# Kernel optimization log

Hardware: AMD Instinct MI355X
Metric: run time of the kernel (lower is better)

## Reference

```python
import jax, jax.numpy as jnp
import numpy as np

B, T, D, H, L = 128, 512, 512, 512, 2

def setup_inputs() -> dict:
    key = jax.random.key(0)
    k1, k2 = jax.random.split(key)
    x = jax.random.normal(k1, (B, T, D), dtype=jnp.float32)
    hiddens = jnp.zeros((L, 2, B, H), dtype=jnp.float32)  # [layer, (h,c), batch, hidden]
    # stacked per-layer fused-gate weights; torch Linear(in+hid, 4*hid)
    W = jax.random.normal(k2, (L, D + H, 4 * H), dtype=jnp.float32) * (1.0 / np.sqrt(D + H))
    b = jnp.zeros((L, 4 * H), dtype=jnp.float32)
    return {"x": x, "hiddens": hiddens, "W": W, "b": b}

def reference(x, hiddens, W, b):
    num_layers = W.shape[0]

    def step(hid, x_t):
        inp = x_t
        new = []
        for l in range(num_layers):
            h, c = hid[l, 0], hid[l, 1]
            gates = jnp.concatenate([inp, h], axis=-1) @ W[l] + b[l]  # [B, 4H]
            i, f, g, o = jnp.split(gates, 4, axis=-1)
            i = jax.nn.sigmoid(i)
            f = jax.nn.sigmoid(f)
            g = jnp.tanh(g)
            o = jax.nn.sigmoid(o)
            c_t = f * c + i * g
            h_t = o * jnp.tanh(c_t)
            new.append(jnp.stack([h_t, c_t], axis=0))
            inp = h_t
        hid = jnp.stack(new, axis=0)
        return hid, inp  # emit top-layer h per timestep

    hiddens_final, outs = jax.lax.scan(step, hiddens, jnp.swapaxes(x, 0, 1))
    outputs = jnp.swapaxes(outs, 0, 1)  # [B, T, H]
    return outputs, hiddens_final
```

## Files before the change

kernel.cpp:

```cpp
#include <hip/hip_runtime.h>
#include <stdint.h>

typedef __attribute__((ext_vector_type(4))) int   i32x4;
typedef __attribute__((ext_vector_type(8))) short bf16x8;
typedef __attribute__((ext_vector_type(4))) float f32x4;

#define DEV static __device__ __forceinline__

constexpr int  kB = 128, kT = 512, kD = 512, kH = 512;
constexpr int  kGC = 2048;
constexpr int  ROWS = 32;
constexpr int  NG = 4;
constexpr int  NJ = 32;
constexpr int  NTHREADS = 512;
constexpr size_t SLOT_ELEMS = (size_t)kB * kH;
constexpr size_t WIMG_ELEMS = (size_t)2 * NJ * 4 * 32 * 512;
constexpr size_t WIMG_BYTES = WIMG_ELEMS * 2;
constexpr int  RFULL = kT + 1;
constexpr int  FLAG_STRIDE = 128;
constexpr size_t FLAG_TOTAL = (size_t)2 * NG * kT * FLAG_STRIDE;
constexpr uint64_t ONE8 = 0x0101010101010101ull;

DEV ushort f2bf(float f) {
  uint32_t u = __float_as_uint(f);
  u += 0x7fff + ((u >> 16) & 1);
  return (ushort)(u >> 16);
}
DEV int pk2(float a, float b) { return (int)((uint32_t)f2bf(a) | ((uint32_t)f2bf(b) << 16)); }
DEV float sigf(float v)  { return 1.f / (1.f + __expf(-v)); }
DEV float tanhf_(float v){ return 1.f - 2.f / (__expf(2.f * v) + 1.f); }

DEV uint64_t ald64(const uint64_t* p) {
  return __hip_atomic_load(p, __ATOMIC_RELAXED, __HIP_MEMORY_SCOPE_AGENT);
}

DEV void poll32(const uint8_t* fb) {
  const uint64_t* p = reinterpret_cast<const uint64_t*>(fb);
  for (;;) {
    uint64_t a = ald64(p) & ald64(p + 1) & ald64(p + 2) & ald64(p + 3);
    if (a == ONE8) return;
    __builtin_amdgcn_s_sleep(1);
  }
}

__global__ void prep_w(const float* __restrict__ W, ushort* __restrict__ wimg) {
  uint32_t idx = blockIdx.x * 256u + threadIdx.x;
  int e = idx & 7, lane = (idx >> 3) & 63, ks = (idx >> 9) & 31;
  int G = (idx >> 14) & 3, j = (idx >> 16) & 31, l = (idx >> 21) & 1;
  int k = ks * 32 + ((lane >> 4) << 3) + e;
  int c = G * 512 + j * 16 + (lane & 15);
  wimg[idx] = f2bf(W[(size_t)l * 1024 * 2048 + (size_t)k * 2048 + c]);
}

__global__ void prep_init(const float* __restrict__ hiddens, ushort* __restrict__ r0, ushort* __restrict__ r1) {
  uint32_t idx = blockIdx.x * 256u + threadIdx.x;
  int l = idx >> 16; uint32_t r = idx & 65535u;
  ushort v = f2bf(hiddens[(size_t)(l * 2 + 0) * 65536 + r]);
  (l ? r1 : r0)[r] = v;
}

DEV void stage_h(ushort* Ab, const ushort* rbase, int g, int tid) {
  #pragma unroll
  for (int p = 0; p < 4; ++p) {
    int o = (tid + p * NTHREADS) * 16, row = o >> 10, kb = o & 1023;
    i32x4 v = *reinterpret_cast<const i32x4*>(rbase + (size_t)(g * ROWS + row) * kH + (kb >> 1));
    *reinterpret_cast<i32x4*>(reinterpret_cast<char*>(Ab) + ((row * 1024 + kb) ^ ((row & 7) << 4))) = v;
  }
}

DEV int gsw(int r, int c) { return r * 16 + (c ^ ((((r) >> 2) & 3) << 2)); }

__launch_bounds__(NTHREADS, 1)
__global__ void lstm_v7(const float* __restrict__ x, const float* __restrict__ hiddens,
                        const float* __restrict__ bias, const ushort* __restrict__ wimg,
                        ushort* __restrict__ ring0, ushort* __restrict__ ring1,
                        uint8_t* __restrict__ flags, float* __restrict__ out) {
  __shared__ ushort AbufX[ROWS * 512];
  __shared__ ushort AbufH[ROWS * 512];
  __shared__ float  gbuf[4][4][ROWS * 16];

  const int tid  = threadIdx.x;
  const int lane = tid & 63;
  const int wv   = tid >> 6;
  const int kq   = wv >> 1;
  const int Gp   = wv & 1;
  const int j    = blockIdx.x & 31;
  const int g    = (blockIdx.x >> 5) & 3;
  const int l    = blockIdx.x >> 7;

  __threadfence();

  i32x4 wrA[8], wrB[8];
  {
    const int GA = 2 * Gp, GB = 2 * Gp + 1;
    const ushort* baseA = wimg + (((size_t)(l * NJ + j) * 4 + GA) * 32) * 512 + lane * 8;
    const ushort* baseB = wimg + (((size_t)(l * NJ + j) * 4 + GB) * 32) * 512 + lane * 8;
    #pragma unroll
    for (int s = 0; s < 4; ++s) {
      wrA[s]     = *reinterpret_cast<const i32x4*>(baseA + (kq * 4 + s) * 512);
      wrA[4 + s] = *reinterpret_cast<const i32x4*>(baseA + (16 + kq * 4 + s) * 512);
      wrB[s]     = *reinterpret_cast<const i32x4*>(baseB + (kq * 4 + s) * 512);
      wrB[4 + s] = *reinterpret_cast<const i32x4*>(baseB + (16 + kq * 4 + s) * 512);
    }
  }
  const int urow = tid >> 4, ucol = tid & 15;
  const float b0 = bias[l * kGC + 0 * 512 + j * 16 + ucol];
  const float b1 = bias[l * kGC + 1 * 512 + j * 16 + ucol];
  const float b2 = bias[l * kGC + 2 * 512 + j * 16 + ucol];
  const float b3 = bias[l * kGC + 3 * 512 + j * 16 + ucol];
  float creg = hiddens[((size_t)(l * 2 + 1) * kB + (g * ROWS + urow)) * kH + j * 16 + ucol];

  ushort* rrec = l ? ring1 : ring0;
  uint8_t* myflags = flags + (size_t)(l * NG + g) * kT * FLAG_STRIDE;
  const uint8_t* xflags = flags + (size_t)g * kT * FLAG_STRIDE;

  const int koff   = (lane >> 4) << 3;
  const int abase0 = (lane & 15) * 1024;
  const int abase1 = abase0 + 16 * 1024;
  const int aswz   = (lane & 7) << 4;
  const int uswz   = gsw(urow, ucol);

  f32x4 xr[8];
  if (l == 0) {
    #pragma unroll
    for (int p = 0; p < 4; ++p) {
      int o = (tid + p * NTHREADS) * 16, row = o >> 10, kb = o & 1023;
      const float* src = x + ((size_t)(g * ROWS + row) * kT + 0) * kD + (kb >> 1);
      xr[2 * p]     = *reinterpret_cast<const f32x4*>(src);
      xr[2 * p + 1] = *reinterpret_cast<const f32x4*>(src + 4);
    }
  }

  for (int t = 0; t < kT; ++t) {
    if (l == 0) {
      #pragma unroll
      for (int p = 0; p < 4; ++p) {
        int o = (tid + p * NTHREADS) * 16, row = o >> 10, kb = o & 1023;
        i32x4 v;
        v[0] = pk2(xr[2 * p][0], xr[2 * p][1]);         v[1] = pk2(xr[2 * p][2], xr[2 * p][3]);
        v[2] = pk2(xr[2 * p + 1][0], xr[2 * p + 1][1]); v[3] = pk2(xr[2 * p + 1][2], xr[2 * p + 1][3]);
        *reinterpret_cast<i32x4*>(reinterpret_cast<char*>(AbufX) + ((row * 1024 + kb) ^ ((row & 7) << 4))) = v;
      }
    } else {
      poll32(xflags + (size_t)t * FLAG_STRIDE);
      stage_h(AbufX, ring0 + (size_t)(t + 1) * SLOT_ELEMS, g, tid);
    }
    __syncthreads();

    if (l == 0 && t + 1 < kT) {
      #pragma unroll
      for (int p = 0; p < 4; ++p) {
        int o = (tid + p * NTHREADS) * 16, row = o >> 10, kb = o & 1023;
        const float* src = x + ((size_t)(g * ROWS + row) * kT + (t + 1)) * kD + (kb >> 1);
        xr[2 * p]     = *reinterpret_cast<const f32x4*>(src);
        xr[2 * p + 1] = *reinterpret_cast<const f32x4*>(src + 4);
      }
    }

    f32x4 a0r0 = {}, a0r1 = {}, a1r0 = {}, a1r1 = {};
    #pragma unroll
    for (int s = 0; s < 4; ++s) {
      int kb = ((kq * 4 + s) * 32 + koff) << 1;
      i32x4 av0 = *reinterpret_cast<const i32x4*>(reinterpret_cast<const char*>(AbufX) + ((abase0 + kb) ^ aswz));
      i32x4 av1 = *reinterpret_cast<const i32x4*>(reinterpret_cast<const char*>(AbufX) + ((abase1 + kb) ^ aswz));
      a0r0 = __builtin_amdgcn_mfma_f32_16x16x32_bf16(
               *reinterpret_cast<bf16x8*>(&av0), *reinterpret_cast<bf16x8*>(&wrA[s]), a0r0, 0, 0, 0);
      a1r0 = __builtin_amdgcn_mfma_f32_16x16x32_bf16(
               *reinterpret_cast<bf16x8*>(&av0), *reinterpret_cast<bf16x8*>(&wrB[s]), a1r0, 0, 0, 0);
      a0r1 = __builtin_amdgcn_mfma_f32_16x16x32_bf16(
               *reinterpret_cast<bf16x8*>(&av1), *reinterpret_cast<bf16x8*>(&wrA[s]), a0r1, 0, 0, 0);
      a1r1 = __builtin_amdgcn_mfma_f32_16x16x32_bf16(
               *reinterpret_cast<bf16x8*>(&av1), *reinterpret_cast<bf16x8*>(&wrB[s]), a1r1, 0, 0, 0);
    }

    if (t > 0) poll32(myflags + (size_t)(t - 1) * FLAG_STRIDE);
    stage_h(AbufH, rrec + (size_t)t * SLOT_ELEMS, g, tid);
    __syncthreads();

    #pragma unroll
    for (int s = 0; s < 4; ++s) {
      int kb = ((kq * 4 + s) * 32 + koff) << 1;
      i32x4 av0 = *reinterpret_cast<const i32x4*>(reinterpret_cast<const char*>(AbufH) + ((abase0 + kb) ^ aswz));
      i32x4 av1 = *reinterpret_cast<const i32x4*>(reinterpret_cast<const char*>(AbufH) + ((abase1 + kb) ^ aswz));
      a0r0 = __builtin_amdgcn_mfma_f32_16x16x32_bf16(
               *reinterpret_cast<bf16x8*>(&av0), *reinterpret_cast<bf16x8*>(&wrA[4 + s]), a0r0, 0, 0, 0);
      a1r0 = __builtin_amdgcn_mfma_f32_16x16x32_bf16(
               *reinterpret_cast<bf16x8*>(&av0), *reinterpret_cast<bf16x8*>(&wrB[4 + s]), a1r0, 0, 0, 0);
      a0r1 = __builtin_amdgcn_mfma_f32_16x16x32_bf16(
               *reinterpret_cast<bf16x8*>(&av1), *reinterpret_cast<bf16x8*>(&wrA[4 + s]), a0r1, 0, 0, 0);
      a1r1 = __builtin_amdgcn_mfma_f32_16x16x32_bf16(
               *reinterpret_cast<bf16x8*>(&av1), *reinterpret_cast<bf16x8*>(&wrB[4 + s]), a1r1, 0, 0, 0);
    }

    #pragma unroll
    for (int q = 0; q < 4; ++q) {
      int r0 = ((lane >> 4) << 2) + q;
      int c  = lane & 15;
      gbuf[kq][2 * Gp + 0][gsw(r0, c)]      = a0r0[q];
      gbuf[kq][2 * Gp + 1][gsw(r0, c)]      = a1r0[q];
      gbuf[kq][2 * Gp + 0][gsw(r0 + 16, c)] = a0r1[q];
      gbuf[kq][2 * Gp + 1][gsw(r0 + 16, c)] = a1r1[q];
    }
    __syncthreads();

    float hh;
    {
      float si = gbuf[0][0][uswz] + gbuf[1][0][uswz] + gbuf[2][0][uswz] + gbuf[3][0][uswz];
      float sf = gbuf[0][1][uswz] + gbuf[1][1][uswz] + gbuf[2][1][uswz] + gbuf[3][1][uswz];
      float sg = gbuf[0][2][uswz] + gbuf[1][2][uswz] + gbuf[2][2][uswz] + gbuf[3][2][uswz];
      float so = gbuf[0][3][uswz] + gbuf[1][3][uswz] + gbuf[2][3][uswz] + gbuf[3][3][uswz];
      float iv = sigf(si + b0);
      float fv = sigf(sf + b1);
      float gv = tanhf_(sg + b2);
      float ov = sigf(so + b3);
      creg = fv * creg + iv * gv;
      hh = ov * tanhf_(creg);
      uint32_t me    = f2bf(hh);
      uint32_t other = (uint32_t)__shfl_xor((int)me, 1);
      if (!(ucol & 1)) {
        uint32_t pkv = me | (other << 16);
        uint32_t* dst = (uint32_t*)(rrec + (size_t)(t + 1) * SLOT_ELEMS
                                    + (size_t)(g * ROWS + urow) * kH + j * 16 + ucol);
        __hip_atomic_store(dst, pkv, __ATOMIC_RELAXED, __HIP_MEMORY_SCOPE_AGENT);
      }
    }
    asm volatile("s_waitcnt vmcnt(0)" ::: "memory");
    __syncthreads();
    if (tid == 0)
      __hip_atomic_store(myflags + (size_t)t * FLAG_STRIDE + j, (uint8_t)1,
                         __ATOMIC_RELAXED, __HIP_MEMORY_SCOPE_AGENT);

    {
      int b = g * ROWS + urow;
      if (l == 1) out[((size_t)b * kT + t) * kH + j * 16 + ucol] = hh;
      if (t == kT - 1) {
        size_t hb = (size_t)kB * kT * kH;
        out[hb + ((size_t)(l * 2 + 0) * kB + b) * kH + j * 16 + ucol] = hh;
        out[hb + ((size_t)(l * 2 + 1) * kB + b) * kH + j * 16 + ucol] = creg;
      }
    }
  }
}


template<bool BIG>
DEV void stage_ring(ushort* Abuf_, const ushort* rbase, int g, int tid) {
  #pragma unroll
  for (int p = 0; p < 4; ++p) {
    int o = (tid + p * NTHREADS) * 16;
    int row = o >> 10, kb = o & 1023;
    const ushort* src = rbase + (size_t)(g * ROWS + row) * kH + (kb >> 1);
    i32x4 v;
    if (BIG) {
      v = *reinterpret_cast<const i32x4*>(src);
    } else {
      uint64_t lo = __hip_atomic_load((const uint64_t*)src,       __ATOMIC_RELAXED, __HIP_MEMORY_SCOPE_AGENT);
      uint64_t hi = __hip_atomic_load((const uint64_t*)(src + 4), __ATOMIC_RELAXED, __HIP_MEMORY_SCOPE_AGENT);
      v[0] = (int)(uint32_t)lo; v[1] = (int)(uint32_t)(lo >> 32);
      v[2] = (int)(uint32_t)hi; v[3] = (int)(uint32_t)(hi >> 32);
    }
    *reinterpret_cast<i32x4*>(reinterpret_cast<char*>(Abuf_) + ((row * 1024 + kb) ^ ((row & 7) << 4))) = v;
  }
}

template<bool BIG>
__launch_bounds__(NTHREADS, 2)
__global__ void lstm_main(const float* __restrict__ x, const float* __restrict__ hiddens,
                          const float* __restrict__ bias, const ushort* __restrict__ wimg,
                          ushort* __restrict__ ring0, ushort* __restrict__ ring1,
                          int* __restrict__ cnt, int* __restrict__ cons0,
                          float* __restrict__ out, int R0, int R1) {
  __shared__ ushort Abuf[ROWS * 512];
  __shared__ float  gbuf[4][ROWS][16];
  __shared__ float  cbuf[ROWS][16];
  __shared__ float  hbuf[ROWS][16];

  const int tid  = threadIdx.x;
  const int lane = tid & 63;
  const int wv   = tid >> 6;
  const int G    = wv & 3;
  const int rf   = wv >> 2;
  const int j    = blockIdx.x & 31;
  const int g    = (blockIdx.x >> 5) & 3;
  const int l    = blockIdx.x >> 7;

  __threadfence();

  i32x4 wr[32];
  {
    const ushort* base = wimg + (((size_t)(l * NJ + j) * 4 + G) * 32) * 512 + lane * 8;
    #pragma unroll
    for (int ks = 0; ks < 32; ++ks)
      wr[ks] = *reinterpret_cast<const i32x4*>(base + ks * 512);
  }
  const float bval = bias[l * kGC + G * 512 + j * 16 + (lane & 15)];
  {
    int row = tid >> 4, col = tid & 15;
    cbuf[row][col] = hiddens[((size_t)(l * 2 + 1) * kB + (g * ROWS + row)) * kH + j * 16 + col];
  }
  int* mycnt = cnt + (l * NG + g) * kT;
  int* c0cnt = cnt + g * kT;
  ushort* rrec = l ? ring1 : ring0;
  const int Rrec = l ? R1 : R0;

  const int arow  = rf * 16 + (lane & 15);
  const int koff  = (lane >> 4) << 3;
  const int abase = arow * 1024;
  const int aswz  = (arow & 7) << 4;

  __syncthreads();

  for (int t = 0; t < kT; ++t) {
    if (l == 1) {
      if (tid == 0) {
        while (__hip_atomic_load(&c0cnt[t], __ATOMIC_RELAXED, __HIP_MEMORY_SCOPE_AGENT) < NJ)
          __builtin_amdgcn_s_sleep(2);
      }
      __syncthreads();
      stage_ring<BIG>(Abuf, ring0 + (size_t)((t + 1) % R0) * SLOT_ELEMS, g, tid);
    } else {
      #pragma unroll
      for (int p = 0; p < 4; ++p) {
        int o = (tid + p * NTHREADS) * 16;
        int row = o >> 10, kb = o & 1023;
        const float* src = x + ((size_t)(g * ROWS + row) * kT + t) * kD + (kb >> 1);
        f32x4 f0 = *reinterpret_cast<const f32x4*>(src);
        f32x4 f1 = *reinterpret_cast<const f32x4*>(src + 4);
        i32x4 v;
        v[0] = pk2(f0[0], f0[1]); v[1] = pk2(f0[2], f0[3]);
        v[2] = pk2(f1[0], f1[1]); v[3] = pk2(f1[2], f1[3]);
        *reinterpret_cast<i32x4*>(reinterpret_cast<char*>(Abuf) + ((row * 1024 + kb) ^ ((row & 7) << 4))) = v;
      }
    }
    __syncthreads();
    if (!BIG && l == 1 && tid == 0)
      __hip_atomic_fetch_add(&cons0[g * kT + t], 1, __ATOMIC_RELAXED, __HIP_MEMORY_SCOPE_AGENT);

    f32x4 acc = {};
    #pragma unroll
    for (int ks = 0; ks < 16; ++ks) {
      int off = (abase + ((ks * 32 + koff) << 1)) ^ aswz;
      i32x4 av = *reinterpret_cast<const i32x4*>(reinterpret_cast<const char*>(Abuf) + off);
      acc = __builtin_amdgcn_mfma_f32_16x16x32_bf16(
              *reinterpret_cast<bf16x8*>(&av), *reinterpret_cast<bf16x8*>(&wr[ks]), acc, 0, 0, 0);
    }
    __syncthreads();

    if (t > 0) {
      if (tid == 0) {
        while (__hip_atomic_load(&mycnt[t - 1], __ATOMIC_RELAXED, __HIP_MEMORY_SCOPE_AGENT) < NJ)
          __builtin_amdgcn_s_sleep(2);
        if (!BIG && l == 0 && t >= R0) {
          while (__hip_atomic_load(&cons0[g * kT + (t - R0)], __ATOMIC_RELAXED, __HIP_MEMORY_SCOPE_AGENT) < NJ)
            __builtin_amdgcn_s_sleep(2);
        }
      }
      __syncthreads();
    }
    stage_ring<BIG>(Abuf, rrec + (size_t)(t % Rrec) * SLOT_ELEMS, g, tid);
    __syncthreads();

    #pragma unroll
    for (int ks = 0; ks < 16; ++ks) {
      int off = (abase + ((ks * 32 + koff) << 1)) ^ aswz;
      i32x4 av = *reinterpret_cast<const i32x4*>(reinterpret_cast<const char*>(Abuf) + off);
      acc = __builtin_amdgcn_mfma_f32_16x16x32_bf16(
              *reinterpret_cast<bf16x8*>(&av), *reinterpret_cast<bf16x8*>(&wr[16 + ks]), acc, 0, 0, 0);
    }

    #pragma unroll
    for (int q = 0; q < 4; ++q) {
      float v2 = acc[q] + bval;
      v2 = (G == 2) ? tanhf_(v2) : sigf(v2);
      gbuf[G][rf * 16 + ((lane >> 4) << 2) + q][lane & 15] = v2;
    }
    __syncthreads();

    {
      int row = tid >> 4, col = tid & 15;
      float iv = gbuf[0][row][col], fv = gbuf[1][row][col];
      float gv = gbuf[2][row][col], ov = gbuf[3][row][col];
      float cc = fv * cbuf[row][col] + iv * gv;
      cbuf[row][col] = cc;
      float hh = ov * tanhf_(cc);
      hbuf[row][col] = hh;
      int b = g * ROWS + row;
      if (l == 1) out[((size_t)b * kT + t) * kH + j * 16 + col] = hh;
      if (t == kT - 1) {
        size_t hb = (size_t)kB * kT * kH;
        out[hb + ((size_t)(l * 2 + 0) * kB + b) * kH + j * 16 + col] = hh;
        out[hb + ((size_t)(l * 2 + 1) * kB + b) * kH + j * 16 + col] = cc;
      }
    }
    __syncthreads();

    if (tid < 256) {
      int row = tid >> 3, cp = tid & 7;
      uint32_t pkv = (uint32_t)f2bf(hbuf[row][2 * cp]) | ((uint32_t)f2bf(hbuf[row][2 * cp + 1]) << 16);
      uint32_t* dst = (uint32_t*)(rrec + (size_t)((t + 1) % Rrec) * SLOT_ELEMS
                                  + (size_t)(g * ROWS + row) * kH + j * 16 + 2 * cp);
      __hip_atomic_store(dst, pkv, __ATOMIC_RELAXED, __HIP_MEMORY_SCOPE_AGENT);
    }
    asm volatile("s_waitcnt vmcnt(0)" ::: "memory");
    __syncthreads();
    if (tid == 0)
      __hip_atomic_fetch_add(&mycnt[t], 1, __ATOMIC_RELAXED, __HIP_MEMORY_SCOPE_AGENT);
  }
}

extern "C" void kernel_launch(void* const* d_in, const int* in_sizes, int n_in,
                              void* d_out, int out_size, void* d_ws, size_t ws_size,
                              hipStream_t stream) {
  const float* x  = (const float*)d_in[0];
  const float* hd = (const float*)d_in[1];
  const float* W  = (const float*)d_in[2];
  const float* b  = (const float*)d_in[3];
  float* out = (float*)d_out;

  char* ws = (char*)d_ws;
  ushort* wimg = (ushort*)ws;
  uint8_t* flags = (uint8_t*)(ws + WIMG_BYTES);
  int* cnt  = (int*)(ws + WIMG_BYTES + FLAG_TOTAL);
  int* cons = (int*)(ws + WIMG_BYTES + FLAG_TOTAL + 16384);
  size_t ringoff = WIMG_BYTES + FLAG_TOTAL + 32768;
  size_t avail = ws_size > ringoff ? ws_size - ringoff : 0;
  long rmax = (long)(avail / (2 * SLOT_ELEMS * 2));
  int R = (rmax >= RFULL) ? RFULL : (rmax >= 16 ? 16 : (rmax >= 2 ? (int)rmax : 2));
  ushort* ring0 = (ushort*)(ws + ringoff);
  ushort* ring1 = ring0 + (size_t)R * SLOT_ELEMS;

  prep_w<<<(int)(WIMG_ELEMS / 256), 256, 0, stream>>>(W, wimg);
  prep_init<<<(2 * kB * kH) / 256, 256, 0, stream>>>(hd, ring0, ring1);
  if (R == RFULL) {
    hipMemsetAsync(flags, 0, FLAG_TOTAL, stream);
    lstm_v7<<<256, NTHREADS, 0, stream>>>(x, hd, b, wimg, ring0, ring1, flags, out);
  } else {
    hipMemsetAsync(ws + WIMG_BYTES + FLAG_TOTAL, 0, 32768, stream);
    lstm_main<false><<<256, NTHREADS, 0, stream>>>(x, hd, b, wimg, ring0, ring1, cnt, cons, out, R, R);
  }
}
```

Measured before the change: 2.160 ms.

## Split batch into 16-row groups, doubling persistent blocks to 512

Batch groups shrink from 32 to 16 rows, giving 8 groups per layer and 512 persistent blocks instead of 256. Each block does half the MFMA and staging work per step, which shortens the per-timestep critical path on the serial recurrence. The cost is that every block loads the same register-resident weights, so weight traffic doubles, and flag synchronisation fans out more widely. Half the threads sit idle in the elementwise phase. The persistent scheme also needs all 512 blocks co-resident, which the launch bound of four blocks per CU is meant to allow.

```diff
diff --git a/kernel.cpp b/kernel.cpp
--- a/kernel.cpp
+++ b/kernel.cpp
@@ -10,7 +10,9 @@
 constexpr int  kB = 128, kT = 512, kD = 512, kH = 512;
 constexpr int  kGC = 2048;
 constexpr int  ROWS = 32;
+constexpr int  GROWS = 16;
 constexpr int  NG = 4;
+constexpr int  NGG = 8;
 constexpr int  NJ = 32;
 constexpr int  NTHREADS = 512;
 constexpr size_t SLOT_ELEMS = (size_t)kB * kH;
@@ -18,7 +20,7 @@
 constexpr size_t WIMG_BYTES = WIMG_ELEMS * 2;
 constexpr int  RFULL = kT + 1;
 constexpr int  FLAG_STRIDE = 128;
-constexpr size_t FLAG_TOTAL = (size_t)2 * NG * kT * FLAG_STRIDE;
+constexpr size_t FLAG_TOTAL = (size_t)2 * NGG * kT * FLAG_STRIDE;
 constexpr uint64_t ONE8 = 0x0101010101010101ull;
 
 DEV ushort f2bf(float f) {
@@ -59,25 +61,25 @@
   (l ? r1 : r0)[r] = v;
 }
 
-DEV void stage_h(ushort* Ab, const ushort* rbase, int g, int tid) {
+DEV void stage_h16(ushort* Ab, const ushort* rbase, int gg, int tid) {
   #pragma unroll
-  for (int p = 0; p < 4; ++p) {
+  for (int p = 0; p < 2; ++p) {
     int o = (tid + p * NTHREADS) * 16, row = o >> 10, kb = o & 1023;
-    i32x4 v = *reinterpret_cast<const i32x4*>(rbase + (size_t)(g * ROWS + row) * kH + (kb >> 1));
+    i32x4 v = *reinterpret_cast<const i32x4*>(rbase + (size_t)(gg * GROWS + row) * kH + (kb >> 1));
     *reinterpret_cast<i32x4*>(reinterpret_cast<char*>(Ab) + ((row * 1024 + kb) ^ ((row & 7) << 4))) = v;
   }
 }
 
 DEV int gsw(int r, int c) { return r * 16 + (c ^ ((((r) >> 2) & 3) << 2)); }
 
-__launch_bounds__(NTHREADS, 1)
-__global__ void lstm_v7(const float* __restrict__ x, const float* __restrict__ hiddens,
+__launch_bounds__(NTHREADS, 4)
+__global__ void lstm_v8(const float* __restrict__ x, const float* __restrict__ hiddens,
                         const float* __restrict__ bias, const ushort* __restrict__ wimg,
                         ushort* __restrict__ ring0, ushort* __restrict__ ring1,
                         uint8_t* __restrict__ flags, float* __restrict__ out) {
-  __shared__ ushort AbufX[ROWS * 512];
-  __shared__ ushort AbufH[ROWS * 512];
-  __shared__ float  gbuf[4][4][ROWS * 16];
+  __shared__ ushort AbufX[GROWS * 512];
+  __shared__ ushort AbufH[GROWS * 512];
+  __shared__ float  gbuf[4][4][GROWS * 16];
 
   const int tid  = threadIdx.x;
   const int lane = tid & 63;
@@ -85,8 +87,8 @@
   const int kq   = wv >> 1;
   const int Gp   = wv & 1;
   const int j    = blockIdx.x & 31;
-  const int g    = (blockIdx.x >> 5) & 3;
-  const int l    = blockIdx.x >> 7;
+  const int gg   = (blockIdx.x >> 5) & 7;
+  const int l    = blockIdx.x >> 8;
 
   __threadfence();
 
@@ -103,29 +105,31 @@
       wrB[4 + s] = *reinterpret_cast<const i32x4*>(baseB + (16 + kq * 4 + s) * 512);
     }
   }
-  const int urow = tid >> 4, ucol = tid & 15;
-  const float b0 = bias[l * kGC + 0 * 512 + j * 16 + ucol];
-  const float b1 = bias[l * kGC + 1 * 512 + j * 16 + ucol];
-  const float b2 = bias[l * kGC + 2 * 512 + j * 16 + ucol];
-  const float b3 = bias[l * kGC + 3 * 512 + j * 16 + ucol];
-  float creg = hiddens[((size_t)(l * 2 + 1) * kB + (g * ROWS + urow)) * kH + j * 16 + ucol];
+  const int urow = (tid >> 4) & 15, ucol = tid & 15;
+  float b0 = 0.f, b1 = 0.f, b2 = 0.f, b3 = 0.f, creg = 0.f;
+  if (tid < 256) {
+    b0 = bias[l * kGC + 0 * 512 + j * 16 + ucol];
+    b1 = bias[l * kGC + 1 * 512 + j * 16 + ucol];
+    b2 = bias[l * kGC + 2 * 512 + j * 16 + ucol];
+    b3 = bias[l * kGC + 3 * 512 + j * 16 + ucol];
+    creg = hiddens[((size_t)(l * 2 + 1) * kB + (gg * GROWS + urow)) * kH + j * 16 + ucol];
+  }
 
   ushort* rrec = l ? ring1 : ring0;
-  uint8_t* myflags = flags + (size_t)(l * NG + g) * kT * FLAG_STRIDE;
-  const uint8_t* xflags = flags + (size_t)g * kT * FLAG_STRIDE;
-
-  const int koff   = (lane >> 4) << 3;
-  const int abase0 = (lane & 15) * 1024;
-  const int abase1 = abase0 + 16 * 1024;
-  const int aswz   = (lane & 7) << 4;
-  const int uswz   = gsw(urow, ucol);
-
-  f32x4 xr[8];
+  uint8_t* myflags = flags + (size_t)(l * NGG + gg) * kT * FLAG_STRIDE;
+  const uint8_t* xflags = flags + (size_t)gg * kT * FLAG_STRIDE;
+
+  const int koff  = (lane >> 4) << 3;
+  const int abase = (lane & 15) * 1024;
+  const int aswz  = (lane & 7) << 4;
+  const int uswz  = gsw(urow, ucol);
+
+  f32x4 xr[4];
   if (l == 0) {
     #pragma unroll
-    for (int p = 0; p < 4; ++p) {
+    for (int p = 0; p < 2; ++p) {
       int o = (tid + p * NTHREADS) * 16, row = o >> 10, kb = o & 1023;
-      const float* src = x + ((size_t)(g * ROWS + row) * kT + 0) * kD + (kb >> 1);
+      const float* src = x + ((size_t)(gg * GROWS + row) * kT + 0) * kD + (kb >> 1);
       xr[2 * p]     = *reinterpret_cast<const f32x4*>(src);
       xr[2 * p + 1] = *reinterpret_cast<const f32x4*>(src + 4);
     }
@@ -134,7 +138,7 @@
   for (int t = 0; t < kT; ++t) {
     if (l == 0) {
       #pragma unroll
-      for (int p = 0; p < 4; ++p) {
+      for (int p = 0; p < 2; ++p) {
         int o = (tid + p * NTHREADS) * 16, row = o >> 10, kb = o & 1023;
         i32x4 v;
         v[0] = pk2(xr[2 * p][0], xr[2 * p][1]);         v[1] = pk2(xr[2 * p][2], xr[2 * p][3]);
@@ -143,68 +147,55 @@
       }
     } else {
       poll32(xflags + (size_t)t * FLAG_STRIDE);
-      stage_h(AbufX, ring0 + (size_t)(t + 1) * SLOT_ELEMS, g, tid);
+      stage_h16(AbufX, ring0 + (size_t)(t + 1) * SLOT_ELEMS, gg, tid);
     }
     __syncthreads();
 
     if (l == 0 && t + 1 < kT) {
       #pragma unroll
-      for (int p = 0; p < 4; ++p) {
+      for (int p = 0; p < 2; ++p) {
         int o = (tid + p * NTHREADS) * 16, row = o >> 10, kb = o & 1023;
-        const float* src = x + ((size_t)(g * ROWS + row) * kT + (t + 1)) * kD + (kb >> 1);
+        const float* src = x + ((size_t)(gg * GROWS + row) * kT + (t + 1)) * kD + (kb >> 1);
         xr[2 * p]     = *reinterpret_cast<const f32x4*>(src);
         xr[2 * p + 1] = *reinterpret_cast<const f32x4*>(src + 4);
       }
     }
 
-    f32x4 a0r0 = {}, a0r1 = {}, a1r0 = {}, a1r1 = {};
+    f32x4 a0 = {}, a1 = {};
     #pragma unroll
     for (int s = 0; s < 4; ++s) {
       int kb = ((kq * 4 + s) * 32 + koff) << 1;
-      i32x4 av0 = *reinterpret_cast<const i32x4*>(reinterpret_cast<const char*>(AbufX) + ((abase0 + kb) ^ aswz));
-      i32x4 av1 = *reinterpret_cast<const i32x4*>(reinterpret_cast<const char*>(AbufX) + ((abase1 + kb) ^ aswz));
-      a0r0 = __builtin_amdgcn_mfma_f32_16x16x32_bf16(
-               *reinterpret_cast<bf16x8*>(&av0), *reinterpret_cast<bf16x8*>(&wrA[s]), a0r0, 0, 0, 0);
-      a1r0 = __builtin_amdgcn_mfma_f32_16x16x32_bf16(
-               *reinterpret_cast<bf16x8*>(&av0), *reinterpret_cast<bf16x8*>(&wrB[s]), a1r0, 0, 0, 0);
-      a0r1 = __builtin_amdgcn_mfma_f32_16x16x32_bf16(
-               *reinterpret_cast<bf16x8*>(&av1), *reinterpret_cast<bf16x8*>(&wrA[s]), a0r1, 0, 0, 0);
-      a1r1 = __builtin_amdgcn_mfma_f32_16x16x32_bf16(
-               *reinterpret_cast<bf16x8*>(&av1), *reinterpret_cast<bf16x8*>(&wrB[s]), a1r1, 0, 0, 0);
+      i32x4 av = *reinterpret_cast<const i32x4*>(reinterpret_cast<const char*>(AbufX) + ((abase + kb) ^ aswz));
+      a0 = __builtin_amdgcn_mfma_f32_16x16x32_bf16(
+             *reinterpret_cast<bf16x8*>(&av), *reinterpret_cast<bf16x8*>(&wrA[s]), a0, 0, 0, 0);
+      a1 = __builtin_amdgcn_mfma_f32_16x16x32_bf16(
+             *reinterpret_cast<bf16x8*>(&av), *reinterpret_cast<bf16x8*>(&wrB[s]), a1, 0, 0, 0);
     }
 
     if (t > 0) poll32(myflags + (size_t)(t - 1) * FLAG_STRIDE);
-    stage_h(AbufH, rrec + (size_t)t * SLOT_ELEMS, g, tid);
+    stage_h16(AbufH, rrec + (size_t)t * SLOT_ELEMS, gg, tid);
     __syncthreads();
 
     #pragma unroll
     for (int s = 0; s < 4; ++s) {
       int kb = ((kq * 4 + s) * 32 + koff) << 1;
-      i32x4 av0 = *reinterpret_cast<const i32x4*>(reinterpret_cast<const char*>(AbufH) + ((abase0 + kb) ^ aswz));
-      i32x4 av1 = *reinterpret_cast<const i32x4*>(reinterpret_cast<const char*>(AbufH) + ((abase1 + kb) ^ aswz));
-      a0r0 = __builtin_amdgcn_mfma_f32_16x16x32_bf16(
-               *reinterpret_cast<bf16x8*>(&av0), *reinterpret_cast<bf16x8*>(&wrA[4 + s]), a0r0, 0, 0, 0);
-      a1r0 = __builtin_amdgcn_mfma_f32_16x16x32_bf16(
-               *reinterpret_cast<bf16x8*>(&av0), *reinterpret_cast<bf16x8*>(&wrB[4 + s]), a1r0, 0, 0, 0);
-      a0r1 = __builtin_amdgcn_mfma_f32_16x16x32_bf16(
-               *reinterpret_cast<bf16x8*>(&av1), *reinterpret_cast<bf16x8*>(&wrA[4 + s]), a0r1, 0, 0, 0);
-      a1r1 = __builtin_amdgcn_mfma_f32_16x16x32_bf16(
-               *reinterpret_cast<bf16x8*>(&av1), *reinterpret_cast<bf16x8*>(&wrB[4 + s]), a1r1, 0, 0, 0);
+      i32x4 av = *reinterpret_cast<const i32x4*>(reinterpret_cast<const char*>(AbufH) + ((abase + kb) ^ aswz));
+      a0 = __builtin_amdgcn_mfma_f32_16x16x32_bf16(
+             *reinterpret_cast<bf16x8*>(&av), *reinterpret_cast<bf16x8*>(&wrA[4 + s]), a0, 0, 0, 0);
+      a1 = __builtin_amdgcn_mfma_f32_16x16x32_bf16(
+             *reinterpret_cast<bf16x8*>(&av), *reinterpret_cast<bf16x8*>(&wrB[4 + s]), a1, 0, 0, 0);
     }
 
     #pragma unroll
     for (int q = 0; q < 4; ++q) {
-      int r0 = ((lane >> 4) << 2) + q;
-      int c  = lane & 15;
-      gbuf[kq][2 * Gp + 0][gsw(r0, c)]      = a0r0[q];
-      gbuf[kq][2 * Gp + 1][gsw(r0, c)]      = a1r0[q];
-      gbuf[kq][2 * Gp + 0][gsw(r0 + 16, c)] = a0r1[q];
-      gbuf[kq][2 * Gp + 1][gsw(r0 + 16, c)] = a1r1[q];
-    }
-    __syncthreads();
-
-    float hh;
-    {
+      int r = ((lane >> 4) << 2) + q, c = lane & 15;
+      gbuf[kq][2 * Gp + 0][gsw(r, c)] = a0[q];
+      gbuf[kq][2 * Gp + 1][gsw(r, c)] = a1[q];
+    }
+    __syncthreads();
+
+    float hh = 0.f;
+    if (tid < 256) {
       float si = gbuf[0][0][uswz] + gbuf[1][0][uswz] + gbuf[2][0][uswz] + gbuf[3][0][uswz];
       float sf = gbuf[0][1][uswz] + gbuf[1][1][uswz] + gbuf[2][1][uswz] + gbuf[3][1][uswz];
       float sg = gbuf[0][2][uswz] + gbuf[1][2][uswz] + gbuf[2][2][uswz] + gbuf[3][2][uswz];
@@ -220,7 +211,7 @@
       if (!(ucol & 1)) {
         uint32_t pkv = me | (other << 16);
         uint32_t* dst = (uint32_t*)(rrec + (size_t)(t + 1) * SLOT_ELEMS
-                                    + (size_t)(g * ROWS + urow) * kH + j * 16 + ucol);
+                                    + (size_t)(gg * GROWS + urow) * kH + j * 16 + ucol);
         __hip_atomic_store(dst, pkv, __ATOMIC_RELAXED, __HIP_MEMORY_SCOPE_AGENT);
       }
     }
@@ -230,8 +221,8 @@
       __hip_atomic_store(myflags + (size_t)t * FLAG_STRIDE + j, (uint8_t)1,
                          __ATOMIC_RELAXED, __HIP_MEMORY_SCOPE_AGENT);
 
-    {
-      int b = g * ROWS + urow;
+    if (tid < 256) {
+      int b = gg * GROWS + urow;
       if (l == 1) out[((size_t)b * kT + t) * kH + j * 16 + ucol] = hh;
       if (t == kT - 1) {
         size_t hb = (size_t)kB * kT * kH;
@@ -433,7 +424,7 @@
   prep_init<<<(2 * kB * kH) / 256, 256, 0, stream>>>(hd, ring0, ring1);
   if (R == RFULL) {
     hipMemsetAsync(flags, 0, FLAG_TOTAL, stream);
-    lstm_v7<<<256, NTHREADS, 0, stream>>>(x, hd, b, wimg, ring0, ring1, flags, out);
+    lstm_v8<<<512, NTHREADS, 0, stream>>>(x, hd, b, wimg, ring0, ring1, flags, out);
   } else {
     hipMemsetAsync(ws + WIMG_BYTES + FLAG_TOTAL, 0, 32768, stream);
     lstm_main<false><<<256, NTHREADS, 0, stream>>>(x, hd, b, wimg, ring0, ring1, cnt, cons, out, R, R);
```

New measurement: 2.331 ms. +7.9%, slower.

## Load MFMA A-operands directly from global into registers, dropping LDS staging

Applied to the files above, without the earlier changes.

Each wave now reads its own x and h MFMA fragments straight from global memory (the ring buffers or x) into registers, instead of the whole block cooperatively staging them into swizzled LDS buffers. This removes two __syncthreads per timestep along with the LDS write/read round trip on the serial recurrence path. In exchange each wave issues smaller, less coalesced global loads (16-byte chunks at row stride), there is redundant loading across waves sharing rows, and register pressure rises because of the larger x prefetch array.

```diff
diff --git a/kernel.cpp b/kernel.cpp
--- a/kernel.cpp
+++ b/kernel.cpp
@@ -59,25 +59,14 @@
   (l ? r1 : r0)[r] = v;
 }
 
-DEV void stage_h(ushort* Ab, const ushort* rbase, int g, int tid) {
-  #pragma unroll
-  for (int p = 0; p < 4; ++p) {
-    int o = (tid + p * NTHREADS) * 16, row = o >> 10, kb = o & 1023;
-    i32x4 v = *reinterpret_cast<const i32x4*>(rbase + (size_t)(g * ROWS + row) * kH + (kb >> 1));
-    *reinterpret_cast<i32x4*>(reinterpret_cast<char*>(Ab) + ((row * 1024 + kb) ^ ((row & 7) << 4))) = v;
-  }
-}
-
 DEV int gsw(int r, int c) { return r * 16 + (c ^ ((((r) >> 2) & 3) << 2)); }
 
 __launch_bounds__(NTHREADS, 1)
-__global__ void lstm_v7(const float* __restrict__ x, const float* __restrict__ hiddens,
+__global__ void lstm_v9(const float* __restrict__ x, const float* __restrict__ hiddens,
                         const float* __restrict__ bias, const ushort* __restrict__ wimg,
                         ushort* __restrict__ ring0, ushort* __restrict__ ring1,
                         uint8_t* __restrict__ flags, float* __restrict__ out) {
-  __shared__ ushort AbufX[ROWS * 512];
-  __shared__ ushort AbufH[ROWS * 512];
-  __shared__ float  gbuf[4][4][ROWS * 16];
+  __shared__ float gbuf[4][4][ROWS * 16];
 
   const int tid  = threadIdx.x;
   const int lane = tid & 63;
@@ -114,92 +103,90 @@
   uint8_t* myflags = flags + (size_t)(l * NG + g) * kT * FLAG_STRIDE;
   const uint8_t* xflags = flags + (size_t)g * kT * FLAG_STRIDE;
 
-  const int koff   = (lane >> 4) << 3;
-  const int abase0 = (lane & 15) * 1024;
-  const int abase1 = abase0 + 16 * 1024;
-  const int aswz   = (lane & 7) << 4;
-  const int uswz   = gsw(urow, ucol);
-
-  f32x4 xr[8];
+  const int r0 = lane & 15;
+  const int cb = (lane >> 4) << 3;
+  const int ksb = kq * 4;
+  const int uswz = gsw(urow, ucol);
+
+  f32x4 xpf[16];
   if (l == 0) {
-    #pragma unroll
-    for (int p = 0; p < 4; ++p) {
-      int o = (tid + p * NTHREADS) * 16, row = o >> 10, kb = o & 1023;
-      const float* src = x + ((size_t)(g * ROWS + row) * kT + 0) * kD + (kb >> 1);
-      xr[2 * p]     = *reinterpret_cast<const f32x4*>(src);
-      xr[2 * p + 1] = *reinterpret_cast<const f32x4*>(src + 4);
+    const float* xb0 = x + ((size_t)(g * ROWS + r0) * kT + 0) * kD + cb;
+    #pragma unroll
+    for (int f = 0; f < 8; ++f) {
+      const float* src = xb0 + (size_t)((f >> 2) * 16) * kT * kD + (ksb + (f & 3)) * 32;
+      xpf[2 * f]     = *reinterpret_cast<const f32x4*>(src);
+      xpf[2 * f + 1] = *reinterpret_cast<const f32x4*>(src + 4);
     }
   }
 
   for (int t = 0; t < kT; ++t) {
+    i32x4 xb[8];
     if (l == 0) {
       #pragma unroll
-      for (int p = 0; p < 4; ++p) {
-        int o = (tid + p * NTHREADS) * 16, row = o >> 10, kb = o & 1023;
+      for (int f = 0; f < 8; ++f) {
         i32x4 v;
-        v[0] = pk2(xr[2 * p][0], xr[2 * p][1]);         v[1] = pk2(xr[2 * p][2], xr[2 * p][3]);
-        v[2] = pk2(xr[2 * p + 1][0], xr[2 * p + 1][1]); v[3] = pk2(xr[2 * p + 1][2], xr[2 * p + 1][3]);
-        *reinterpret_cast<i32x4*>(reinterpret_cast<char*>(AbufX) + ((row * 1024 + kb) ^ ((row & 7) << 4))) = v;
+        v[0] = pk2(xpf[2 * f][0], xpf[2 * f][1]);         v[1] = pk2(xpf[2 * f][2], xpf[2 * f][3]);
+        v[2] = pk2(xpf[2 * f + 1][0], xpf[2 * f + 1][1]); v[3] = pk2(xpf[2 * f + 1][2], xpf[2 * f + 1][3]);
+        xb[f] = v;
+      }
+      if (t + 1 < kT) {
+        const float* xb0 = x + ((size_t)(g * ROWS + r0) * kT + (t + 1)) * kD + cb;
+        #pragma unroll
+        for (int f = 0; f < 8; ++f) {
+          const float* src = xb0 + (size_t)((f >> 2) * 16) * kT * kD + (ksb + (f & 3)) * 32;
+          xpf[2 * f]     = *reinterpret_cast<const f32x4*>(src);
+          xpf[2 * f + 1] = *reinterpret_cast<const f32x4*>(src + 4);
+        }
       }
     } else {
       poll32(xflags + (size_t)t * FLAG_STRIDE);
-      stage_h(AbufX, ring0 + (size_t)(t + 1) * SLOT_ELEMS, g, tid);
-    }
-    __syncthreads();
-
-    if (l == 0 && t + 1 < kT) {
+      const ushort* xs = ring0 + (size_t)(t + 1) * SLOT_ELEMS + (size_t)(g * ROWS + r0) * kH + cb;
       #pragma unroll
-      for (int p = 0; p < 4; ++p) {
-        int o = (tid + p * NTHREADS) * 16, row = o >> 10, kb = o & 1023;
-        const float* src = x + ((size_t)(g * ROWS + row) * kT + (t + 1)) * kD + (kb >> 1);
-        xr[2 * p]     = *reinterpret_cast<const f32x4*>(src);
-        xr[2 * p + 1] = *reinterpret_cast<const f32x4*>(src + 4);
-      }
+      for (int f = 0; f < 8; ++f)
+        xb[f] = *reinterpret_cast<const i32x4*>(xs + (size_t)((f >> 2) * 16) * kH + (ksb + (f & 3)) * 32);
     }
 
     f32x4 a0r0 = {}, a0r1 = {}, a1r0 = {}, a1r1 = {};
     #pragma unroll
     for (int s = 0; s < 4; ++s) {
-      int kb = ((kq * 4 + s) * 32 + koff) << 1;
-      i32x4 av0 = *reinterpret_cast<const i32x4*>(reinterpret_cast<const char*>(AbufX) + ((abase0 + kb) ^ aswz));
-      i32x4 av1 = *reinterpret_cast<const i32x4*>(reinterpret_cast<const char*>(AbufX) + ((abase1 + kb) ^ aswz));
       a0r0 = __builtin_amdgcn_mfma_f32_16x16x32_bf16(
-               *reinterpret_cast<bf16x8*>(&av0), *reinterpret_cast<bf16x8*>(&wrA[s]), a0r0, 0, 0, 0);
+               *reinterpret_cast<bf16x8*>(&xb[s]), *reinterpret_cast<bf16x8*>(&wrA[s]), a0r0, 0, 0, 0);
       a1r0 = __builtin_amdgcn_mfma_f32_16x16x32_bf16(
-               *reinterpret_cast<bf16x8*>(&av0), *reinterpret_cast<bf16x8*>(&wrB[s]), a1r0, 0, 0, 0);
+               *reinterpret_cast<bf16x8*>(&xb[s]), *reinterpret_cast<bf16x8*>(&wrB[s]), a1r0, 0, 0, 0);
       a0r1 = __builtin_amdgcn_mfma_f32_16x16x32_bf16(
-               *reinterpret_cast<bf16x8*>(&av1), *reinterpret_cast<bf16x8*>(&wrA[s]), a0r1, 0, 0, 0);
+               *reinterpret_cast<bf16x8*>(&xb[4 + s]), *reinterpret_cast<bf16x8*>(&wrA[s]), a0r1, 0, 0, 0);
       a1r1 = __builtin_amdgcn_mfma_f32_16x16x32_bf16(
-               *reinterpret_cast<bf16x8*>(&av1), *reinterpret_cast<bf16x8*>(&wrB[s]), a1r1, 0, 0, 0);
+               *reinterpret_cast<bf16x8*>(&xb[4 + s]), *reinterpret_cast<bf16x8*>(&wrB[s]), a1r1, 0, 0, 0);
     }
 
     if (t > 0) poll32(myflags + (size_t)(t - 1) * FLAG_STRIDE);
-    stage_h(AbufH, rrec + (size_t)t * SLOT_ELEMS, g, tid);
-    __syncthreads();
+    i32x4 hr[8];
+    {
+      const ushort* hs = rrec + (size_t)t * SLOT_ELEMS + (size_t)(g * ROWS + r0) * kH + cb;
+      #pragma unroll
+      for (int f = 0; f < 8; ++f)
+        hr[f] = *reinterpret_cast<const i32x4*>(hs + (size_t)((f >> 2) * 16) * kH + (ksb + (f & 3)) * 32);
+    }
 
     #pragma unroll
     for (int s = 0; s < 4; ++s) {
-      int kb = ((kq * 4 + s) * 32 + koff) << 1;
-      i32x4 av0 = *reinterpret_cast<const i32x4*>(reinterpret_cast<const char*>(AbufH) + ((abase0 + kb) ^ aswz));
-      i32x4 av1 = *reinterpret_cast<const i32x4*>(reinterpret_cast<const char*>(AbufH) + ((abase1 + kb) ^ aswz));
       a0r0 = __builtin_amdgcn_mfma_f32_16x16x32_bf16(
-               *reinterpret_cast<bf16x8*>(&av0), *reinterpret_cast<bf16x8*>(&wrA[4 + s]), a0r0, 0, 0, 0);
+               *reinterpret_cast<bf16x8*>(&hr[s]), *reinterpret_cast<bf16x8*>(&wrA[4 + s]), a0r0, 0, 0, 0);
       a1r0 = __builtin_amdgcn_mfma_f32_16x16x32_bf16(
-               *reinterpret_cast<bf16x8*>(&av0), *reinterpret_cast<bf16x8*>(&wrB[4 + s]), a1r0, 0, 0, 0);
+               *reinterpret_cast<bf16x8*>(&hr[s]), *reinterpret_cast<bf16x8*>(&wrB[4 + s]), a1r0, 0, 0, 0);
       a0r1 = __builtin_amdgcn_mfma_f32_16x16x32_bf16(
-               *reinterpret_cast<bf16x8*>(&av1), *reinterpret_cast<bf16x8*>(&wrA[4 + s]), a0r1, 0, 0, 0);
+               *reinterpret_cast<bf16x8*>(&hr[4 + s]), *reinterpret_cast<bf16x8*>(&wrA[4 + s]), a0r1, 0, 0, 0);
       a1r1 = __builtin_amdgcn_mfma_f32_16x16x32_bf16(
-               *reinterpret_cast<bf16x8*>(&av1), *reinterpret_cast<bf16x8*>(&wrB[4 + s]), a1r1, 0, 0, 0);
+               *reinterpret_cast<bf16x8*>(&hr[4 + s]), *reinterpret_cast<bf16x8*>(&wrB[4 + s]), a1r1, 0, 0, 0);
     }
 
     #pragma unroll
     for (int q = 0; q < 4; ++q) {
-      int r0 = ((lane >> 4) << 2) + q;
-      int c  = lane & 15;
-      gbuf[kq][2 * Gp + 0][gsw(r0, c)]      = a0r0[q];
-      gbuf[kq][2 * Gp + 1][gsw(r0, c)]      = a1r0[q];
-      gbuf[kq][2 * Gp + 0][gsw(r0 + 16, c)] = a0r1[q];
-      gbuf[kq][2 * Gp + 1][gsw(r0 + 16, c)] = a1r1[q];
+      int rr = ((lane >> 4) << 2) + q, c = lane & 15;
+      gbuf[kq][2 * Gp + 0][gsw(rr, c)]      = a0r0[q];
+      gbuf[kq][2 * Gp + 1][gsw(rr, c)]      = a1r0[q];
+      gbuf[kq][2 * Gp + 0][gsw(rr + 16, c)] = a0r1[q];
+      gbuf[kq][2 * Gp + 1][gsw(rr + 16, c)] = a1r1[q];
     }
     __syncthreads();
 
@@ -433,7 +420,7 @@
   prep_init<<<(2 * kB * kH) / 256, 256, 0, stream>>>(hd, ring0, ring1);
   if (R == RFULL) {
     hipMemsetAsync(flags, 0, FLAG_TOTAL, stream);
-    lstm_v7<<<256, NTHREADS, 0, stream>>>(x, hd, b, wimg, ring0, ring1, flags, out);
+    lstm_v9<<<256, NTHREADS, 0, stream>>>(x, hd, b, wimg, ring0, ring1, flags, out);
   } else {
     hipMemsetAsync(ws + WIMG_BYTES + FLAG_TOTAL, 0, 32768, stream);
     lstm_main<false><<<256, NTHREADS, 0, stream>>>(x, hd, b, wimg, ring0, ring1, cnt, cons, out, R, R);
```

Result: slower. 4.095 ms (+89.6%).
